# Performance work log

Measured on AMD Instinct MI355X. Metric: run time of the kernel, lower is better.

The kernel has to match this reference:

```python
import jax, jax.numpy as jnp
import numpy as np
import math

N_EMBD = 512
N_BRANCH = 4
BLOCK = 2048
B, T = 2, 2048


def make_rope_tables(dim, max_len):
    inv_freq = 1.0 / (10000.0 ** (np.arange(0, dim, 2, dtype=np.float32) / dim))
    t = np.arange(max_len, dtype=np.float32)
    freqs = np.einsum('i,j->ij', t, inv_freq)  # [max_len, dim/2]
    return jnp.asarray(np.cos(freqs)), jnp.asarray(np.sin(freqs))


def apply_rope(xq, cos, sin):
    # xq: [..., T, C]; cos/sin: [T, C/2]
    x1 = xq[..., 0::2]
    x2 = xq[..., 1::2]
    y1 = x1 * cos - x2 * sin
    y2 = x1 * sin + x2 * cos
    return jnp.stack((y1, y2), axis=-1).reshape(xq.shape)


def setup_inputs() -> dict:
    key = jax.random.key(0)
    ks = jax.random.split(key, 6)
    C, NB = N_EMBD, N_BRANCH
    s = 1.0 / math.sqrt(C)
    a = jax.random.normal(ks[0], (B, T, C), jnp.float32)
    x = jax.random.normal(ks[1], (B, T, C), jnp.float32)
    Wq = jax.random.normal(ks[2], (C, C * NB), jnp.float32) * s
    Wk = jax.random.normal(ks[3], (C, C), jnp.float32) * s
    Wv = jax.random.normal(ks[4], (C, C * NB), jnp.float32) * s
    Wo = jax.random.normal(ks[5], (C, C), jnp.float32) * s
    cos, sin = make_rope_tables(C, BLOCK)
    return {"a": a, "x": x, "Wq": Wq, "Wk": Wk, "Wv": Wv, "Wo": Wo,
            "cos": cos, "sin": sin}


def reference(a, x, Wq, Wk, Wv, Wo, cos, sin):
    Bb, Tt, C = x.shape
    NB = Wq.shape[1] // C
    cos_t = cos[:Tt]
    sin_t = sin[:Tt]

    q = (a @ Wq).reshape(Bb, Tt, NB, C).transpose(0, 2, 1, 3)  # [B,NB,T,C]
    v = (a @ Wv).reshape(Bb, Tt, NB, C).transpose(0, 2, 1, 3)  # [B,NB,T,C]
    k = (x @ Wk)[:, None, :, :]                                # [B,1,T,C]

    q = apply_rope(q, cos_t, sin_t)
    k = apply_rope(k, cos_t, sin_t)

    att = jnp.einsum('bntc,bosc->bnts', q, k) / math.sqrt(C)   # [B,NB,T,T]
    causal = jnp.tril(jnp.ones((Tt, Tt), bool))                # [T,T]
    att_m = jnp.where(causal, att, -jnp.inf)

    # softmax over branch axis; mask is identical across branches, so compute
    # on unmasked logits and zero-out masked positions (== nan_to_num of
    # softmax over fully -inf columns)
    soft_probs = jnp.where(causal, jax.nn.softmax(att, axis=1), 0.0)

    max_val = jnp.max(soft_probs, axis=1, keepdims=True)
    hard_mask = jax.lax.stop_gradient((soft_probs == max_val).astype(att.dtype))
    route_mask = jax.lax.stop_gradient(hard_mask - soft_probs) + soft_probs

    att_max = jnp.max(att_m, axis=1)                           # [B,T,T]
    attn_probs = jax.nn.softmax(att_max, axis=-1)              # [B,T,T]

    combined = attn_probs[:, None, :, :] * route_mask          # [B,NB,T,T]
    y = jnp.einsum('bnts,bnsc->btc', combined, v)              # [B,T,C]
    return y @ Wo
```

## Files before the change

kernel.cpp:

```cpp
#include <hip/hip_runtime.h>
#include <math.h>


#define B_ 2
#define T_ 2048
#define C_ 512
#define NB_ 4
#define C2_ 1024

typedef unsigned short u16;
typedef unsigned char u8;
using short8 = __attribute__((ext_vector_type(8))) short;
using bf16x8 = __attribute__((ext_vector_type(8))) __bf16;
using f32x4  = __attribute__((ext_vector_type(4))) float;

__device__ __forceinline__ float bf2f(u16 u) {
  union { unsigned int i; float f; } v; v.i = ((unsigned int)u) << 16; return v.f;
}
__device__ __forceinline__ u16 f2bf(float f) {
  union { float f; unsigned int i; } v; v.f = f;
  unsigned int u = v.i;
  return (u16)((u + 0x7fffu + ((u >> 16) & 1u)) >> 16);
}
__device__ __forceinline__ f32x4 mfma16x16x32(short8 a, short8 b, f32x4 c) {
  return __builtin_amdgcn_mfma_f32_16x16x32_bf16(
      __builtin_bit_cast(bf16x8, a), __builtin_bit_cast(bf16x8, b), c, 0, 0, 0);
}
__device__ __forceinline__ void split8(const float* s, uint4& hi, uint4& lo) {
  u16 h[8], l[8];
#pragma unroll
  for (int j = 0; j < 8; ++j) {
    h[j] = f2bf(s[j]);
    l[j] = f2bf(s[j] - bf2f(h[j]));
  }
  hi.x = h[0] | ((unsigned)h[1] << 16); hi.y = h[2] | ((unsigned)h[3] << 16);
  hi.z = h[4] | ((unsigned)h[5] << 16); hi.w = h[6] | ((unsigned)h[7] << 16);
  lo.x = l[0] | ((unsigned)l[1] << 16); lo.y = l[2] | ((unsigned)l[3] << 16);
  lo.z = l[4] | ((unsigned)l[5] << 16); lo.w = l[6] | ((unsigned)l[7] << 16);
}
__device__ __forceinline__ int swz(int row) { return ((row >> 1) & 3) << 3; }

template <int MODE>
__global__ __launch_bounds__(256) void gemm_qk(const float* __restrict__ A,
                                               const float* __restrict__ W,
                                               u16* __restrict__ out,
                                               const float* __restrict__ cosT,
                                               const float* __restrict__ sinT,
                                               const int N, const int K) {
  __shared__ u16 Ah[64][32], Al[64][32];
  __shared__ u16 Bh[64][32], Bl[64][32];
  const int tid = threadIdx.x;
  const int wave = tid >> 6, lane = tid & 63;
  const int m0 = blockIdx.y << 6, n0 = blockIdx.x << 6;
  const f32x4 zero = {0.f, 0.f, 0.f, 0.f};
  f32x4 acc[4] = {zero, zero, zero, zero};
  const int srow = tid >> 2, koff = ((tid & 3) << 3) ^ swz(tid >> 2);
  const int lrow = lane & 15, lk = ((lane >> 4) << 3) ^ swz(lane & 15);
  for (int kk = 0; kk < K; kk += 32) {
    const int kg = (tid & 3) << 3;
    float av[8];
    *(float4*)(av) = *(const float4*)(&A[(size_t)(m0 + srow) * K + kk + kg]);
    *(float4*)(av + 4) =
        *(const float4*)(&A[(size_t)(m0 + srow) * K + kk + kg + 4]);
    uint4 hi, lo;
    split8(av, hi, lo);
    *(uint4*)(&Ah[srow][koff]) = hi;
    *(uint4*)(&Al[srow][koff]) = lo;
    float wv[8];
#pragma unroll
    for (int j = 0; j < 8; ++j)
      wv[j] = W[(size_t)(kk + kg + j) * N + n0 + srow];
    split8(wv, hi, lo);
    *(uint4*)(&Bh[srow][koff]) = hi;
    *(uint4*)(&Bl[srow][koff]) = lo;
    __syncthreads();
    short8 ah = *(const short8*)(&Ah[(wave << 4) + lrow][lk]);
    short8 al = *(const short8*)(&Al[(wave << 4) + lrow][lk]);
#pragma unroll
    for (int ns = 0; ns < 4; ++ns) {
      short8 bh = *(const short8*)(&Bh[(ns << 4) + lrow][lk]);
      short8 bl = *(const short8*)(&Bl[(ns << 4) + lrow][lk]);
      acc[ns] = mfma16x16x32(ah, bh, acc[ns]);
      acc[ns] = mfma16x16x32(al, bh, acc[ns]);
      acc[ns] = mfma16x16x32(ah, bl, acc[ns]);
    }
    __syncthreads();
  }
  const int r0 = m0 + (wave << 4) + ((lane >> 4) << 2);
  const int cb = n0 + (lane & 15);
#pragma unroll
  for (int ns = 0; ns < 4; ++ns) {
#pragma unroll
    for (int r = 0; r < 4; ++r) {
      const int rg = r0 + r;
      const int cg = cb + (ns << 4);
      float v = acc[ns][r];
      float pv = __shfl_xor(v, 1);
      const int t = rg & (T_ - 1);
      const int c = (MODE == 1) ? (cg & (C_ - 1)) : cg;
      const int i = c >> 1;
      const float cf = cosT[(t << 8) + i];
      const float sf = sinT[(t << 8) + i];
      float x1 = (lane & 1) ? pv : v;
      float x2 = (lane & 1) ? v : pv;
      float y = (lane & 1) ? (x1 * sf + x2 * cf) : (x1 * cf - x2 * sf);
      if (MODE == 1) y *= 0.044194173824159216f;
      const u16 hi = f2bf(y);
      const u16 lo = f2bf(y - bf2f(hi));
      size_t rowoff;
      if (MODE == 1) {
        const int b = rg >> 11, n = cg >> 9;
        rowoff = ((size_t)((b * NB_ + n) * T_ + t)) * C2_;
      } else {
        rowoff = (size_t)rg * C2_;
      }
      out[rowoff + c] = hi;
      out[rowoff + C_ + c] = lo;
    }
  }
}

template <int AF32, int OF32>
__global__ __launch_bounds__(256) void gemm_hi(const void* __restrict__ Ap,
                                               const float* __restrict__ W,
                                               void* __restrict__ outp,
                                               const int N, const int K) {
  __shared__ u16 As[64][32];
  __shared__ u16 Bs[64][32];
  const int tid = threadIdx.x;
  const int wave = tid >> 6, lane = tid & 63;
  const int m0 = blockIdx.y << 6, n0 = blockIdx.x << 6;
  const f32x4 zero = {0.f, 0.f, 0.f, 0.f};
  f32x4 acc[4] = {zero, zero, zero, zero};
  const int srow = tid >> 2, koff = ((tid & 3) << 3) ^ swz(tid >> 2);
  const int lrow = lane & 15, lk = ((lane >> 4) << 3) ^ swz(lane & 15);
  for (int kk = 0; kk < K; kk += 32) {
    const int kg = (tid & 3) << 3;
    if (AF32) {
      const float* A = (const float*)Ap;
      float av[8];
      *(float4*)(av) = *(const float4*)(&A[(size_t)(m0 + srow) * K + kk + kg]);
      *(float4*)(av + 4) =
          *(const float4*)(&A[(size_t)(m0 + srow) * K + kk + kg + 4]);
      uint4 hi;
      hi.x = f2bf(av[0]) | ((unsigned)f2bf(av[1]) << 16);
      hi.y = f2bf(av[2]) | ((unsigned)f2bf(av[3]) << 16);
      hi.z = f2bf(av[4]) | ((unsigned)f2bf(av[5]) << 16);
      hi.w = f2bf(av[6]) | ((unsigned)f2bf(av[7]) << 16);
      *(uint4*)(&As[srow][koff]) = hi;
    } else {
      const u16* A = (const u16*)Ap;
      *(uint4*)(&As[srow][koff]) =
          *(const uint4*)(&A[(size_t)(m0 + srow) * K + kk + kg]);
    }
    uint4 hi;
    {
      float w[8];
#pragma unroll
      for (int j = 0; j < 8; ++j)
        w[j] = W[(size_t)(kk + kg + j) * N + n0 + srow];
      hi.x = f2bf(w[0]) | ((unsigned)f2bf(w[1]) << 16);
      hi.y = f2bf(w[2]) | ((unsigned)f2bf(w[3]) << 16);
      hi.z = f2bf(w[4]) | ((unsigned)f2bf(w[5]) << 16);
      hi.w = f2bf(w[6]) | ((unsigned)f2bf(w[7]) << 16);
    }
    *(uint4*)(&Bs[srow][koff]) = hi;
    __syncthreads();
    short8 af = *(const short8*)(&As[(wave << 4) + lrow][lk]);
#pragma unroll
    for (int ns = 0; ns < 4; ++ns) {
      short8 bf = *(const short8*)(&Bs[(ns << 4) + lrow][lk]);
      acc[ns] = mfma16x16x32(af, bf, acc[ns]);
    }
    __syncthreads();
  }
  const int r0 = m0 + (wave << 4) + ((lane >> 4) << 2);
  const int cb = n0 + (lane & 15);
#pragma unroll
  for (int ns = 0; ns < 4; ++ns) {
#pragma unroll
    for (int r = 0; r < 4; ++r) {
      const size_t idx = (size_t)(r0 + r) * N + cb + (ns << 4);
      if (OF32) ((float*)outp)[idx] = acc[ns][r];
      else ((u16*)outp)[idx] = f2bf(acc[ns][r]);
    }
  }
}

__global__ __launch_bounds__(256) void transpose_v_k(const u16* __restrict__ Vraw,
                                                     u16* __restrict__ VT) {
  const int bid = blockIdx.x;
  const int ct = bid & 7;
  const int ttile = (bid >> 3) & 31;
  const int n = (bid >> 8) & 3;
  const int b = bid >> 10;
  __shared__ u16 tile[64][68];
  const int tid = threadIdx.x;
  const int rr = tid >> 4;
  const int cc = (tid & 15) << 2;
  const int t0 = ttile << 6, c0 = ct << 6;
#pragma unroll
  for (int it = 0; it < 4; ++it) {
    const int r = (it << 4) + rr;
    *(ushort4*)(&tile[r][cc]) = *(const ushort4*)(
        &Vraw[((size_t)((b << 11) + t0 + r)) * (NB_ * C_) + n * C_ + c0 + cc]);
  }
  __syncthreads();
#pragma unroll
  for (int it = 0; it < 4; ++it) {
    const int c = (it << 4) + rr;
    ushort4 w;
    w.x = tile[cc + 0][c]; w.y = tile[cc + 1][c];
    w.z = tile[cc + 2][c]; w.w = tile[cc + 3][c];
    *(ushort4*)(&VT[((size_t)((b * NB_ + n) * C_ + c0 + c)) * T_ + t0 + cc]) = w;
  }
}

__global__ __launch_bounds__(256) void scores_k(const u16* __restrict__ Qcat,
                                                const u16* __restrict__ Kcat,
                                                u16* __restrict__ Mout,
                                                u8* __restrict__ Mask) {
  const int tri = blockIdx.x;
  int tt = (int)((sqrtf(8.f * (float)tri + 1.f) - 1.f) * 0.5f);
  while ((tt + 1) * (tt + 2) / 2 <= tri) ++tt;
  while (tt * (tt + 1) / 2 > tri) --tt;
  const int ss = tri - tt * (tt + 1) / 2;
  const int b = blockIdx.y;
  __shared__ __align__(16) u16 Qh[2][NB_][64][32], Ql[2][NB_][64][32];
  __shared__ __align__(16) u16 Kh[2][64][32], Kl[2][64][32];
  const int tid = threadIdx.x;
  const int wave = tid >> 6, lane = tid & 63;
  const int t0 = tt << 6, s0 = ss << 6;
  const f32x4 zero = {0.f, 0.f, 0.f, 0.f};
  f32x4 acc[NB_][4];
  for (int n = 0; n < NB_; ++n)
    for (int j = 0; j < 4; ++j) acc[n][j] = zero;
  const int srow = tid >> 2, kg = (tid & 3) << 3;
  const int lrow = lane & 15, lk = (lane >> 4) << 3;
  const int wrow = wave << 4;
  const size_t qstride = (size_t)T_ * C2_;
  const size_t qbase = ((size_t)(b * NB_ * T_ + t0 + srow)) * C2_ + kg;
  const size_t kbase = ((size_t)((b << 11) + s0 + srow)) * C2_ + kg;

  auto stage_sc = [&](int d, int kko) {
#pragma unroll
    for (int n = 0; n < NB_; ++n) {
      const size_t qb = qbase + (size_t)n * qstride + kko;
      __builtin_amdgcn_global_load_lds(
          (const __attribute__((address_space(1))) void*)&Qcat[qb],
          (__attribute__((address_space(3))) void*)&Qh[d][n][wrow][0], 16, 0, 0);
      __builtin_amdgcn_global_load_lds(
          (const __attribute__((address_space(1))) void*)&Qcat[qb + C_],
          (__attribute__((address_space(3))) void*)&Ql[d][n][wrow][0], 16, 0, 0);
    }
    __builtin_amdgcn_global_load_lds(
        (const __attribute__((address_space(1))) void*)&Kcat[kbase + kko],
        (__attribute__((address_space(3))) void*)&Kh[d][wrow][0], 16, 0, 0);
    __builtin_amdgcn_global_load_lds(
        (const __attribute__((address_space(1))) void*)&Kcat[kbase + kko + C_],
        (__attribute__((address_space(3))) void*)&Kl[d][wrow][0], 16, 0, 0);
  };

  stage_sc(0, 0);
  int cur = 0;
#pragma unroll 2
  for (int kk = 0; kk < C_; kk += 32) {
    if (kk + 32 < C_) {
      stage_sc(cur ^ 1, kk + 32);
      asm volatile("s_waitcnt vmcnt(10)" ::: "memory");
    } else {
      asm volatile("s_waitcnt vmcnt(0)" ::: "memory");
    }
    __builtin_amdgcn_sched_barrier(0);
    __builtin_amdgcn_s_barrier();
    __builtin_amdgcn_sched_barrier(0);
    short8 qh[NB_], ql[NB_];
#pragma unroll
    for (int n = 0; n < NB_; ++n) {
      qh[n] = *(const short8*)(&Qh[cur][n][wrow + lrow][lk]);
      ql[n] = *(const short8*)(&Ql[cur][n][wrow + lrow][lk]);
    }
#pragma unroll
    for (int ns = 0; ns < 4; ++ns) {
      short8 kh = *(const short8*)(&Kh[cur][(ns << 4) + lrow][lk]);
      short8 kl = *(const short8*)(&Kl[cur][(ns << 4) + lrow][lk]);
#pragma unroll
      for (int n = 0; n < NB_; ++n) {
        acc[n][ns] = mfma16x16x32(qh[n], kh, acc[n][ns]);
        acc[n][ns] = mfma16x16x32(ql[n], kh, acc[n][ns]);
        acc[n][ns] = mfma16x16x32(qh[n], kl, acc[n][ns]);
      }
    }
    __builtin_amdgcn_sched_barrier(0);
    asm volatile("" ::: "memory");
    __builtin_amdgcn_s_barrier();
    __builtin_amdgcn_sched_barrier(0);
    cur ^= 1;
  }
  const int tb = t0 + (wave << 4) + ((lane >> 4) << 2);
  const int sb = s0 + (lane & 15);
#pragma unroll
  for (int ns = 0; ns < 4; ++ns) {
#pragma unroll
    for (int r = 0; r < 4; ++r) {
      const int t = tb + r, s = sb + (ns << 4);
      float a0 = acc[0][ns][r], a1 = acc[1][ns][r];
      float a2 = acc[2][ns][r], a3 = acc[3][ns][r];
      float m = fmaxf(fmaxf(a0, a1), fmaxf(a2, a3));
      u8 msk = (u8)((a0 == m) | ((a1 == m) << 1) | ((a2 == m) << 2) |
                    ((a3 == m) << 3));
      if (s > t) { m = -__builtin_inff(); msk = 0; }
      const size_t idx = (size_t)b * T_ * T_ + (size_t)t * T_ + s;
      Mout[idx] = f2bf(m);
      Mask[idx] = msk;
    }
  }
}

__global__ __launch_bounds__(256) void rowstats_k(const u16* __restrict__ Mb,
                                                  float* __restrict__ Rm,
                                                  float* __restrict__ Rz) {
  const int r = (blockIdx.x << 2) + (threadIdx.x >> 6);
  const int lane = threadIdx.x & 63;
  const int b = r >> 11, t = r & (T_ - 1);
  const u16* row = Mb + (size_t)b * T_ * T_ + (size_t)t * T_;
  float m = -__builtin_inff();
  for (int s = lane; s <= t; s += 64) m = fmaxf(m, bf2f(row[s]));
#pragma unroll
  for (int off = 32; off; off >>= 1) m = fmaxf(m, __shfl_xor(m, off));
  float z = 0.f;
  for (int s = lane; s <= t; s += 64) z += expf(bf2f(row[s]) - m);
#pragma unroll
  for (int off = 32; off; off >>= 1) z += __shfl_xor(z, off);
  if (lane == 0) { Rm[r] = m; Rz[r] = 1.f / z; }
}

__global__ __launch_bounds__(256) void pbuild_k(const u16* __restrict__ Mb,
                                                const float* __restrict__ Rm,
                                                const float* __restrict__ Rz,
                                                u16* __restrict__ Pb) {
  const int r = blockIdx.x;
  const float rm = Rm[r], rz = Rz[r];
  const size_t off = ((size_t)r << 11) + (threadIdx.x << 3);
  ushort4 m0 = *(const ushort4*)(&Mb[off]);
  ushort4 m1 = *(const ushort4*)(&Mb[off + 4]);
  u16 o[8];
  o[0] = f2bf(expf(bf2f(m0.x) - rm) * rz);
  o[1] = f2bf(expf(bf2f(m0.y) - rm) * rz);
  o[2] = f2bf(expf(bf2f(m0.z) - rm) * rz);
  o[3] = f2bf(expf(bf2f(m0.w) - rm) * rz);
  o[4] = f2bf(expf(bf2f(m1.x) - rm) * rz);
  o[5] = f2bf(expf(bf2f(m1.y) - rm) * rz);
  o[6] = f2bf(expf(bf2f(m1.z) - rm) * rz);
  o[7] = f2bf(expf(bf2f(m1.w) - rm) * rz);
  uint4 w;
  w.x = o[0] | ((unsigned)o[1] << 16); w.y = o[2] | ((unsigned)o[3] << 16);
  w.z = o[4] | ((unsigned)o[5] << 16); w.w = o[6] | ((unsigned)o[7] << 16);
  *(uint4*)(&Pb[off]) = w;
}

__global__ __launch_bounds__(256) void pv_k(const u16* __restrict__ Pb,
                                            const u8* __restrict__ Mask,
                                            const u16* __restrict__ VT,
                                            u16* __restrict__ Y) {
  const int ypair = blockIdx.x, cblk = blockIdx.y, b = blockIdx.z;
  const int c0 = cblk << 5;
  __shared__ u16 Ps[NB_][64][32];
  __shared__ u16 Vs[NB_][32][32];
  const int tid = threadIdx.x;
  const int wave = tid >> 6, lane = tid & 63;
  const int prow = tid >> 2, soff = (tid & 3) << 3;
  const int psoff = soff ^ swz(prow);
  const int vrow = tid >> 3, vsoff = (tid & 7) << 2;
  const int vcol = ((((tid & 7) >> 1) ^ ((vrow >> 1) & 3)) << 3) |
                   ((tid & 1) << 2);
  const int lrow = lane & 15, lk = ((lane >> 4) << 3) ^ swz(lane & 15);
  const f32x4 zero = {0.f, 0.f, 0.f, 0.f};
  const size_t vrow_base[NB_] = {
      ((size_t)((b * NB_ + 0) * C_ + c0 + vrow)) * T_,
      ((size_t)((b * NB_ + 1) * C_ + c0 + vrow)) * T_,
      ((size_t)((b * NB_ + 2) * C_ + c0 + vrow)) * T_,
      ((size_t)((b * NB_ + 3) * C_ + c0 + vrow)) * T_};

  for (int half = 0; half < 2; ++half) {
    const int tt = half ? (31 - ypair) : ypair;
    const int t0 = tt << 6;
    const int nchunk = (tt + 1) << 1;
    const size_t pro = ((size_t)((b << 11) + t0 + prow)) << 11;
    f32x4 acc[2] = {zero, zero};
    uint4 pu; uint2 mk2; uint2 vv[NB_];
    pu = *(const uint4*)(&Pb[pro + soff]);
    mk2 = *(const uint2*)(&Mask[pro + soff]);
#pragma unroll
    for (int n = 0; n < NB_; ++n)
      vv[n] = *(const uint2*)(&VT[vrow_base[n] + vsoff]);
    for (int ck = 0; ck < nchunk; ++ck) {
      u16 p[8] = {(u16)pu.x, (u16)(pu.x >> 16), (u16)pu.y, (u16)(pu.y >> 16),
                  (u16)pu.z, (u16)(pu.z >> 16), (u16)pu.w, (u16)(pu.w >> 16)};
      u8 mk[8] = {(u8)mk2.x, (u8)(mk2.x >> 8), (u8)(mk2.x >> 16),
                  (u8)(mk2.x >> 24), (u8)mk2.y, (u8)(mk2.y >> 8),
                  (u8)(mk2.y >> 16), (u8)(mk2.y >> 24)};
#pragma unroll
      for (int n = 0; n < NB_; ++n) {
        uint4 wv;
        wv.x = (unsigned)(((mk[0] >> n) & 1) ? p[0] : 0) |
               ((unsigned)(((mk[1] >> n) & 1) ? p[1] : 0) << 16);
        wv.y = (unsigned)(((mk[2] >> n) & 1) ? p[2] : 0) |
               ((unsigned)(((mk[3] >> n) & 1) ? p[3] : 0) << 16);
        wv.z = (unsigned)(((mk[4] >> n) & 1) ? p[4] : 0) |
               ((unsigned)(((mk[5] >> n) & 1) ? p[5] : 0) << 16);
        wv.w = (unsigned)(((mk[6] >> n) & 1) ? p[6] : 0) |
               ((unsigned)(((mk[7] >> n) & 1) ? p[7] : 0) << 16);
        *(uint4*)(&Ps[n][prow][psoff]) = wv;
        *(uint2*)(&Vs[n][vrow][vcol]) = vv[n];
      }
      __syncthreads();
      if (ck + 1 < nchunk) {
        const int sB = (ck + 1) << 5;
        pu = *(const uint4*)(&Pb[pro + sB + soff]);
        mk2 = *(const uint2*)(&Mask[pro + sB + soff]);
#pragma unroll
        for (int n = 0; n < NB_; ++n)
          vv[n] = *(const uint2*)(&VT[vrow_base[n] + sB + vsoff]);
      }
#pragma unroll
      for (int n = 0; n < NB_; ++n) {
        short8 af = *(const short8*)(&Ps[n][(wave << 4) + lrow][lk]);
#pragma unroll
        for (int cs = 0; cs < 2; ++cs) {
          short8 bf = *(const short8*)(&Vs[n][(cs << 4) + lrow][lk]);
          acc[cs] = mfma16x16x32(af, bf, acc[cs]);
        }
      }
      __syncthreads();
    }
    const int tb = t0 + (wave << 4) + ((lane >> 4) << 2);
    const int cbs = c0 + (lane & 15);
#pragma unroll
    for (int cs = 0; cs < 2; ++cs) {
#pragma unroll
      for (int r = 0; r < 4; ++r) {
        Y[(size_t)((b << 11) + tb + r) * C_ + cbs + (cs << 4)] =
            f2bf(acc[cs][r]);
      }
    }
  }
}

extern "C" void kernel_launch(void* const* d_in, const int* in_sizes, int n_in,
                              void* d_out, int out_size, void* d_ws,
                              size_t ws_size, hipStream_t stream) {
  (void)in_sizes; (void)n_in; (void)out_size; (void)ws_size;
  const float* a    = (const float*)d_in[0];
  const float* x    = (const float*)d_in[1];
  const float* Wq   = (const float*)d_in[2];
  const float* Wk   = (const float*)d_in[3];
  const float* Wv   = (const float*)d_in[4];
  const float* Wo   = (const float*)d_in[5];
  const float* cosT = (const float*)d_in[6];
  const float* sinT = (const float*)d_in[7];

  char* w = (char*)d_ws;
  u16* Qcat   = (u16*)(w + 0);
  u16* Kcat   = (u16*)(w + 33554432);
  u16* Vraw   = (u16*)(w + 41943040);
  u16* VT     = (u16*)(w + 58720256);
  u8*  Mask   = (u8*)(w + 75497472);
  float* Rm   = (float*)(w + 83886080);
  float* Rz   = (float*)(w + 83902464);
  u16* Pb     = (u16*)(w + 83918848);
  u16* Mb     = Vraw;
  u16* Y      = Qcat;

  const dim3 blk(256);
  gemm_qk<1><<<dim3(32, 64), blk, 0, stream>>>(a, Wq, Qcat, cosT, sinT, 2048, 512);
  gemm_qk<2><<<dim3(8, 64), blk, 0, stream>>>(x, Wk, Kcat, cosT, sinT, 512, 512);
  gemm_hi<1, 0><<<dim3(32, 64), blk, 0, stream>>>(a, Wv, (void*)Vraw, 2048, 512);
  transpose_v_k<<<dim3(2048), blk, 0, stream>>>(Vraw, VT);
  scores_k<<<dim3(528, 2), blk, 0, stream>>>(Qcat, Kcat, Mb, Mask);
  rowstats_k<<<dim3(1024), blk, 0, stream>>>(Mb, Rm, Rz);
  pbuild_k<<<dim3(4096), blk, 0, stream>>>(Mb, Rm, Rz, Pb);
  pv_k<<<dim3(16, 16, 2), blk, 0, stream>>>(Pb, Mask, VT, Y);
  gemm_hi<0, 1><<<dim3(8, 64), blk, 0, stream>>>(Y, Wo, d_out, 512, 512);
}
```

Measured before the change: 378.8 us.

## Load Q straight into registers in scores kernel, drop Q LDS staging

The scores kernel no longer stages the Q high/low tiles through LDS. Each wave only uses its own 16 Q rows, so it now loads them directly from global memory into registers every k-step, and only K stays double-buffered in LDS. This cuts LDS use from about 80KB to 16KB per block, so launch_bounds is raised to request 4 blocks per CU. The triangular block index is also remapped with a stride-66 swizzle, which spreads the causal tiles across the grid. The trade-off is that Q reads now go through per-lane global loads, with less latency hiding and possible uncoalesced access.

```diff
diff --git a/kernel.cpp b/kernel.cpp
--- a/kernel.cpp
+++ b/kernel.cpp
@@ -216,17 +216,16 @@
   }
 }
 
-__global__ __launch_bounds__(256) void scores_k(const u16* __restrict__ Qcat,
-                                                const u16* __restrict__ Kcat,
-                                                u16* __restrict__ Mout,
-                                                u8* __restrict__ Mask) {
-  const int tri = blockIdx.x;
+__global__ __launch_bounds__(256, 4) void scores_k(const u16* __restrict__ Qcat,
+                                                   const u16* __restrict__ Kcat,
+                                                   u16* __restrict__ Mout,
+                                                   u8* __restrict__ Mask) {
+  const int tri = ((blockIdx.x & 7) * 66) + (blockIdx.x >> 3);
   int tt = (int)((sqrtf(8.f * (float)tri + 1.f) - 1.f) * 0.5f);
   while ((tt + 1) * (tt + 2) / 2 <= tri) ++tt;
   while (tt * (tt + 1) / 2 > tri) --tt;
   const int ss = tri - tt * (tt + 1) / 2;
   const int b = blockIdx.y;
-  __shared__ __align__(16) u16 Qh[2][NB_][64][32], Ql[2][NB_][64][32];
   __shared__ __align__(16) u16 Kh[2][64][32], Kl[2][64][32];
   const int tid = threadIdx.x;
   const int wave = tid >> 6, lane = tid & 63;
@@ -239,20 +238,11 @@
   const int lrow = lane & 15, lk = (lane >> 4) << 3;
   const int wrow = wave << 4;
   const size_t qstride = (size_t)T_ * C2_;
-  const size_t qbase = ((size_t)(b * NB_ * T_ + t0 + srow)) * C2_ + kg;
+  const size_t qb0 =
+      ((size_t)(b * NB_ * T_ + t0 + wrow + lrow)) * C2_ + lk;
   const size_t kbase = ((size_t)((b << 11) + s0 + srow)) * C2_ + kg;
 
-  auto stage_sc = [&](int d, int kko) {
-#pragma unroll
-    for (int n = 0; n < NB_; ++n) {
-      const size_t qb = qbase + (size_t)n * qstride + kko;
-      __builtin_amdgcn_global_load_lds(
-          (const __attribute__((address_space(1))) void*)&Qcat[qb],
-          (__attribute__((address_space(3))) void*)&Qh[d][n][wrow][0], 16, 0, 0);
-      __builtin_amdgcn_global_load_lds(
-          (const __attribute__((address_space(1))) void*)&Qcat[qb + C_],
-          (__attribute__((address_space(3))) void*)&Ql[d][n][wrow][0], 16, 0, 0);
-    }
+  auto stage_k = [&](int d, int kko) {
     __builtin_amdgcn_global_load_lds(
         (const __attribute__((address_space(1))) void*)&Kcat[kbase + kko],
         (__attribute__((address_space(3))) void*)&Kh[d][wrow][0], 16, 0, 0);
@@ -261,25 +251,25 @@
         (__attribute__((address_space(3))) void*)&Kl[d][wrow][0], 16, 0, 0);
   };
 
-  stage_sc(0, 0);
+  stage_k(0, 0);
   int cur = 0;
-#pragma unroll 2
   for (int kk = 0; kk < C_; kk += 32) {
+    if (kk + 32 < C_) stage_k(cur ^ 1, kk + 32);
+    short8 qh[NB_], ql[NB_];
+#pragma unroll
+    for (int n = 0; n < NB_; ++n) {
+      const size_t qb = qb0 + (size_t)n * qstride + kk;
+      qh[n] = *(const short8*)(&Qcat[qb]);
+      ql[n] = *(const short8*)(&Qcat[qb + C_]);
+    }
     if (kk + 32 < C_) {
-      stage_sc(cur ^ 1, kk + 32);
-      asm volatile("s_waitcnt vmcnt(10)" ::: "memory");
+      asm volatile("s_waitcnt vmcnt(2)" ::: "memory");
     } else {
       asm volatile("s_waitcnt vmcnt(0)" ::: "memory");
     }
     __builtin_amdgcn_sched_barrier(0);
     __builtin_amdgcn_s_barrier();
     __builtin_amdgcn_sched_barrier(0);
-    short8 qh[NB_], ql[NB_];
-#pragma unroll
-    for (int n = 0; n < NB_; ++n) {
-      qh[n] = *(const short8*)(&Qh[cur][n][wrow + lrow][lk]);
-      ql[n] = *(const short8*)(&Ql[cur][n][wrow + lrow][lk]);
-    }
 #pragma unroll
     for (int ns = 0; ns < 4; ++ns) {
       short8 kh = *(const short8*)(&Kh[cur][(ns << 4) + lrow][lk]);
```

New measurement: 392.8 us. 1.04x slower.
